# Kernel optimization log

Hardware: AMD Instinct MI355X
Metric: run time of the kernel (lower is better)

The kernel has to match this reference:

```python
import jax, jax.numpy as jnp
import numpy as np

MARGIN = 0.5
TIME_GAP = 10
EPS = 1e-8  # torch cosine_similarity eps


def setup_inputs() -> dict:
    key = jax.random.key(0)
    hidden_states = jax.random.normal(key, (16, 4096, 512), dtype=jnp.float32)
    return {"hidden_states": hidden_states}


def _sim_shift(h, n, k):
    # cosine similarity between time t and t+k for all valid t, all batches
    # h: [B, S, D], n: [B, S] precomputed norms -> returns [B, S-k]
    dots = jnp.sum(h[:, :-k] * h[:, k:], axis=-1)
    denom = jnp.maximum(n[:, :-k] * n[:, k:], EPS)
    return dots / denom


def reference(hidden_states):
    h = hidden_states
    B, S, D = h.shape
    n = jnp.sqrt(jnp.sum(h * h, axis=-1))  # [B, S], computed once

    # adjacent: sum_t mean_b(1 - sim(t, t+1)) / (S-1) == overall mean
    adjacent_loss = jnp.mean(1.0 - _sim_shift(h, n, 1))

    # distant: shifts k in [TIME_GAP, 2*TIME_GAP), t in [0, S-k)
    distant_total = jnp.zeros((), dtype=h.dtype)
    count = 0
    for k in range(TIME_GAP, min(S, 2 * TIME_GAP)):
        sim = _sim_shift(h, n, k)  # [B, S-k]
        # original sums mean-over-batch per (t,k) pair
        distant_total = distant_total + jnp.sum(jnp.mean(jax.nn.relu(MARGIN - sim), axis=0))
        count += S - k
    distant_loss = distant_total / count if count > 0 else jnp.zeros((), dtype=h.dtype)

    return adjacent_loss + distant_loss
```

## Files before the change

kernel.cpp:

```cpp
#include <hip/hip_runtime.h>
#include <math.h>

constexpr int B_ = 16;
constexpr int S_ = 4096;
constexpr int D_ = 512;
constexpr float MARGIN = 0.5f;
constexpr float EPS = 1e-8f;

constexpr int TGR = 64;
constexpr int WPB = 4;
constexpr int NBLK = B_ * S_ / (TGR * WPB);
constexpr int NW   = NBLK * WPB;
constexpr int SPB  = S_ / TGR;

typedef __attribute__((ext_vector_type(8))) short short8;
typedef __attribute__((ext_vector_type(4))) float floatx4;

template <int CTRL>
__device__ __forceinline__ float dpp_add(float x) {
    int m = __builtin_amdgcn_update_dpp(0, __float_as_int(x), CTRL, 0xf, 0xf, true);
    return x + __int_as_float(m);
}
__device__ __forceinline__ float wave_sum63(float x) {
    x = dpp_add<0x111>(x);
    x = dpp_add<0x112>(x);
    x = dpp_add<0x114>(x);
    x = dpp_add<0x118>(x);
    x = dpp_add<0x142>(x);
    x = dpp_add<0x143>(x);
    return x;
}

__device__ __forceinline__ unsigned int pk(float lo, float hi) {
    return __builtin_amdgcn_perm(__float_as_uint(hi), __float_as_uint(lo), 0x07060302u);
}

__global__ __launch_bounds__(256, 1) void tcl_partial(const float* __restrict__ h,
                                                      float* __restrict__ ws) {
    __shared__ float nlds[WPB][96];

    const int tid  = threadIdx.x;
    const int lane = tid & 63;
    const int w    = tid >> 6;

    const int p  = blockIdx.x;
    const int L  = (p & 7) * (NBLK / 8) + (p >> 3);
    const int gw = L * WPB + w;
    const int b  = gw / SPB;
    const int t0 = (gw % SPB) * TGR;

    const int m16 = lane & 15;
    const int q   = lane >> 4;
    const int q8  = q * 8;

    const float* fb[6];
#pragma unroll
    for (int o = 0; o < 6; ++o) {
        int t = t0 + o * 16 + m16;
        if (o == 5 && t > t0 + 82) t = t0 + 82;
        if (t > S_ - 1) t = S_ - 1;
        fb[o] = h + ((size_t)b * S_ + t) * D_ + q8;
    }

    floatx4 acc[14];
#pragma unroll
    for (int j = 0; j < 14; ++j) acc[j] = (floatx4){0.f, 0.f, 0.f, 0.f};

#pragma unroll
    for (int kk = 0; kk < 16; ++kk) {
        short8 f[6];
#pragma unroll
        for (int o = 0; o < 6; ++o) {
            float4 x = *(const float4*)(fb[o] + kk * 32);
            float4 y = *(const float4*)(fb[o] + kk * 32 + 4);
            union { uint4 u4; short8 s8; } cv;
            cv.u4.x = pk(x.x, x.y);
            cv.u4.y = pk(x.z, x.w);
            cv.u4.z = pk(y.x, y.y);
            cv.u4.w = pk(y.z, y.w);
            f[o] = cv.s8;
        }
        acc[0]  = __builtin_amdgcn_mfma_f32_16x16x32_bf16(f[0], f[0], acc[0],  0, 0, 0);
        acc[1]  = __builtin_amdgcn_mfma_f32_16x16x32_bf16(f[0], f[1], acc[1],  0, 0, 0);
        acc[2]  = __builtin_amdgcn_mfma_f32_16x16x32_bf16(f[0], f[2], acc[2],  0, 0, 0);
        acc[3]  = __builtin_amdgcn_mfma_f32_16x16x32_bf16(f[1], f[1], acc[3],  0, 0, 0);
        acc[4]  = __builtin_amdgcn_mfma_f32_16x16x32_bf16(f[1], f[2], acc[4],  0, 0, 0);
        acc[5]  = __builtin_amdgcn_mfma_f32_16x16x32_bf16(f[1], f[3], acc[5],  0, 0, 0);
        acc[6]  = __builtin_amdgcn_mfma_f32_16x16x32_bf16(f[2], f[2], acc[6],  0, 0, 0);
        acc[7]  = __builtin_amdgcn_mfma_f32_16x16x32_bf16(f[2], f[3], acc[7],  0, 0, 0);
        acc[8]  = __builtin_amdgcn_mfma_f32_16x16x32_bf16(f[2], f[4], acc[8],  0, 0, 0);
        acc[9]  = __builtin_amdgcn_mfma_f32_16x16x32_bf16(f[3], f[3], acc[9],  0, 0, 0);
        acc[10] = __builtin_amdgcn_mfma_f32_16x16x32_bf16(f[3], f[4], acc[10], 0, 0, 0);
        acc[11] = __builtin_amdgcn_mfma_f32_16x16x32_bf16(f[3], f[5], acc[11], 0, 0, 0);
        acc[12] = __builtin_amdgcn_mfma_f32_16x16x32_bf16(f[4], f[4], acc[12], 0, 0, 0);
        acc[13] = __builtin_amdgcn_mfma_f32_16x16x32_bf16(f[5], f[5], acc[13], 0, 0, 0);
    }

    const int DJ[6] = {0, 3, 6, 9, 12, 13};
    const int DB[6] = {0, 16, 32, 48, 64, 80};
#pragma unroll
    for (int d = 0; d < 6; ++d) {
#pragma unroll
        for (int r = 0; r < 4; ++r)
            if (q * 4 + r == m16) nlds[w][DB[d] + m16] = sqrtf(acc[DJ[d]][r]);
    }
    __syncthreads();

    const float w1 = 1.0f / ((float)B_ * (float)(S_ - 1));
    const float w2 = 1.0f / ((float)B_ * (float)(10 * S_ - 145));
    const int SA[12] = {0, 0, 0, 16, 16, 16, 32, 32, 32, 48, 48, 48};
    const int SB[12] = {0, 16, 32, 16, 32, 48, 32, 48, 64, 48, 64, 80};
    float local = 0.f;
#pragma unroll
    for (int s2 = 0; s2 < 12; ++s2) {
        const int gcol = SB[s2] + m16;
        if (t0 + gcol < S_) {
            const float nb = nlds[w][gcol];
#pragma unroll
            for (int r = 0; r < 4; ++r) {
                const int grow = SA[s2] + q * 4 + r;
                const int k = gcol - grow;
                if (k == 1 || (k >= 10 && k <= 19)) {
                    const float sim = acc[s2][r] / fmaxf(nlds[w][grow] * nb, EPS);
                    local += (k == 1) ? w1 * (1.0f - sim)
                                      : w2 * fmaxf(MARGIN - sim, 0.f);
                }
            }
        }
    }

    local = wave_sum63(local);
    if (lane == 63) ws[gw] = local;
}

__global__ __launch_bounds__(1024) void tcl_final(const float* __restrict__ ws,
                                                  float* __restrict__ out) {
    float v = 0.f;
    for (int j = threadIdx.x; j < NW; j += 1024) v += ws[j];
    v = wave_sum63(v);
    __shared__ float s[16];
    if ((threadIdx.x & 63) == 63) s[threadIdx.x >> 6] = v;
    __syncthreads();
    if (threadIdx.x == 0) {
        float t = 0.f;
#pragma unroll
        for (int j = 0; j < 16; j++) t += s[j];
        out[0] = t;
    }
}

extern "C" void kernel_launch(void* const* d_in, const int* in_sizes, int n_in,
                              void* d_out, int out_size, void* d_ws, size_t ws_size,
                              hipStream_t stream) {
    const float* h = (const float*)d_in[0];
    float* out = (float*)d_out;
    float* ws = (float*)d_ws;
    tcl_partial<<<NBLK, 256, 0, stream>>>(h, ws);
    tcl_final<<<1, 1024, 0, stream>>>(ws, out);
}
```

Baseline: 198.7 us.

## Split D reduction across wave pairs with LDS combine of MFMA accumulators

Each 64-row strip is now handled by two waves that each cover half of the 512-wide feature dimension. The second wave writes its 14 accumulator tiles to shared memory and the first wave adds them before computing norms and the loss. This doubles the wave count and halves per-wave serial MFMA/load work to expose more memory parallelism and occupancy (launch_bounds raised to 2 blocks). In exchange it adds about 29KB of LDS per block, an extra barrier, and leaves half the waves idle during the epilogue.

```diff
diff --git a/kernel.cpp b/kernel.cpp
--- a/kernel.cpp
+++ b/kernel.cpp
@@ -7,11 +7,12 @@
 constexpr float MARGIN = 0.5f;
 constexpr float EPS = 1e-8f;
 
-constexpr int TGR = 64;
-constexpr int WPB = 4;
-constexpr int NBLK = B_ * S_ / (TGR * WPB);
-constexpr int NW   = NBLK * WPB;
+constexpr int TGR  = 64;
 constexpr int SPB  = S_ / TGR;
+constexpr int NSTR = B_ * SPB;
+constexpr int WPB  = 4;
+constexpr int NBLK = NSTR * 2 / WPB;
+constexpr int NW   = NSTR;
 
 typedef __attribute__((ext_vector_type(8))) short short8;
 typedef __attribute__((ext_vector_type(4))) float floatx4;
@@ -35,23 +36,26 @@
     return __builtin_amdgcn_perm(__float_as_uint(hi), __float_as_uint(lo), 0x07060302u);
 }
 
-__global__ __launch_bounds__(256, 1) void tcl_partial(const float* __restrict__ h,
+__global__ __launch_bounds__(256, 2) void tcl_partial(const float* __restrict__ h,
                                                       float* __restrict__ ws) {
-    __shared__ float nlds[WPB][96];
+    __shared__ float nlds[2][96];
+    __shared__ float red[2][64][57];
 
     const int tid  = threadIdx.x;
     const int lane = tid & 63;
     const int w    = tid >> 6;
+    const int sw   = w >> 1;
+    const int kh   = w & 1;
 
     const int p  = blockIdx.x;
     const int L  = (p & 7) * (NBLK / 8) + (p >> 3);
-    const int gw = L * WPB + w;
-    const int b  = gw / SPB;
-    const int t0 = (gw % SPB) * TGR;
+    const int strip = L * 2 + sw;
+    const int b  = strip >> 6;
+    const int t0 = (strip & (SPB - 1)) * TGR;
 
     const int m16 = lane & 15;
     const int q   = lane >> 4;
-    const int q8  = q * 8;
+    const int col0 = kh * 256 + q * 8;
 
     const float* fb[6];
 #pragma unroll
@@ -59,7 +63,7 @@
         int t = t0 + o * 16 + m16;
         if (o == 5 && t > t0 + 82) t = t0 + 82;
         if (t > S_ - 1) t = S_ - 1;
-        fb[o] = h + ((size_t)b * S_ + t) * D_ + q8;
+        fb[o] = h + ((size_t)b * S_ + t) * D_ + col0;
     }
 
     floatx4 acc[14];
@@ -67,7 +71,7 @@
     for (int j = 0; j < 14; ++j) acc[j] = (floatx4){0.f, 0.f, 0.f, 0.f};
 
 #pragma unroll
-    for (int kk = 0; kk < 16; ++kk) {
+    for (int kk = 0; kk < 8; ++kk) {
         short8 f[6];
 #pragma unroll
         for (int o = 0; o < 6; ++o) {
@@ -96,41 +100,56 @@
         acc[13] = __builtin_amdgcn_mfma_f32_16x16x32_bf16(f[5], f[5], acc[13], 0, 0, 0);
     }
 
-    const int DJ[6] = {0, 3, 6, 9, 12, 13};
-    const int DB[6] = {0, 16, 32, 48, 64, 80};
+    if (kh == 1) {
 #pragma unroll
-    for (int d = 0; d < 6; ++d) {
+        for (int j = 0; j < 14; ++j)
 #pragma unroll
-        for (int r = 0; r < 4; ++r)
-            if (q * 4 + r == m16) nlds[w][DB[d] + m16] = sqrtf(acc[DJ[d]][r]);
+            for (int r = 0; r < 4; ++r) red[sw][lane][j * 4 + r] = acc[j][r];
+    }
+    __syncthreads();
+    if (kh == 0) {
+#pragma unroll
+        for (int j = 0; j < 14; ++j)
+#pragma unroll
+            for (int r = 0; r < 4; ++r) acc[j][r] += red[sw][lane][j * 4 + r];
+
+        const int DJ[6] = {0, 3, 6, 9, 12, 13};
+        const int DB[6] = {0, 16, 32, 48, 64, 80};
+#pragma unroll
+        for (int d = 0; d < 6; ++d) {
+#pragma unroll
+            for (int r = 0; r < 4; ++r)
+                if (q * 4 + r == m16) nlds[sw][DB[d] + m16] = sqrtf(acc[DJ[d]][r]);
+        }
     }
     __syncthreads();
 
-    const float w1 = 1.0f / ((float)B_ * (float)(S_ - 1));
-    const float w2 = 1.0f / ((float)B_ * (float)(10 * S_ - 145));
-    const int SA[12] = {0, 0, 0, 16, 16, 16, 32, 32, 32, 48, 48, 48};
-    const int SB[12] = {0, 16, 32, 16, 32, 48, 32, 48, 64, 48, 64, 80};
-    float local = 0.f;
+    if (kh == 0) {
+        const float w1 = 1.0f / ((float)B_ * (float)(S_ - 1));
+        const float w2 = 1.0f / ((float)B_ * (float)(10 * S_ - 145));
+        const int SA[12] = {0, 0, 0, 16, 16, 16, 32, 32, 32, 48, 48, 48};
+        const int SB[12] = {0, 16, 32, 16, 32, 48, 32, 48, 64, 48, 64, 80};
+        float local = 0.f;
 #pragma unroll
-    for (int s2 = 0; s2 < 12; ++s2) {
-        const int gcol = SB[s2] + m16;
-        if (t0 + gcol < S_) {
-            const float nb = nlds[w][gcol];
+        for (int s2 = 0; s2 < 12; ++s2) {
+            const int gcol = SB[s2] + m16;
+            if (t0 + gcol < S_) {
+                const float nb = nlds[sw][gcol];
 #pragma unroll
-            for (int r = 0; r < 4; ++r) {
-                const int grow = SA[s2] + q * 4 + r;
-                const int k = gcol - grow;
-                if (k == 1 || (k >= 10 && k <= 19)) {
-                    const float sim = acc[s2][r] / fmaxf(nlds[w][grow] * nb, EPS);
-                    local += (k == 1) ? w1 * (1.0f - sim)
-                                      : w2 * fmaxf(MARGIN - sim, 0.f);
+                for (int r = 0; r < 4; ++r) {
+                    const int grow = SA[s2] + q * 4 + r;
+                    const int k = gcol - grow;
+                    if (k == 1 || (k >= 10 && k <= 19)) {
+                        const float sim = acc[s2][r] / fmaxf(nlds[sw][grow] * nb, EPS);
+                        local += (k == 1) ? w1 * (1.0f - sim)
+                                          : w2 * fmaxf(MARGIN - sim, 0.f);
+                    }
                 }
             }
         }
+        local = wave_sum63(local);
+        if (lane == 63) ws[strip] = local;
     }
-
-    local = wave_sum63(local);
-    if (lane == 63) ws[gw] = local;
 }
 
 __global__ __launch_bounds__(1024) void tcl_final(const float* __restrict__ ws,
```

Result: no change. 202.5 us (+1.9%).
